# Kernel optimization log

Hardware: AMD Instinct MI355X
Metric: run time of the kernel (lower is better)

The kernel has to match this reference:

```python
import jax, jax.numpy as jnp
import numpy as np


def setup_inputs() -> dict:
    key = jax.random.key(0)
    k1, k2 = jax.random.split(key)
    B, C_IN, C_OUT, K = 256, 1024, 1024, 16
    curr_input = jax.random.normal(k1, (B, C_IN, K), dtype=jnp.float32)
    weight = jax.random.normal(k2, (C_OUT, C_IN, K), dtype=jnp.float32)
    return {"curr_input": curr_input, "weight": weight}


def reference(curr_input, weight):
    # Steady-state streaming conv step:
    # output[b, o] = sum_{c,k} curr_input[b, c, k] * weight[o, c, k]
    # This is exactly the triple nested torch.dot loop, fused into one contraction.
    return jnp.einsum("bck,ock->bo", curr_input, weight)
```

## Files before the change

kernel.cpp:

```cpp
#include <hip/hip_runtime.h>
#include <hip/hip_bf16.h>


#define CO    1024
#define KTOT  16384
#define BM    256
#define BN    128
#define NB    8
#define SKB   64
#define KC    (KTOT / SKB)
#define BK    32
#define KITERS (KC / BK)
#define LDA   40
#define SLICE_ELEMS (BM * CO)

typedef __attribute__((ext_vector_type(8))) short short8;
typedef __attribute__((ext_vector_type(4))) float f32x4;
typedef __attribute__((ext_vector_type(4))) unsigned short u16x4;

__device__ __forceinline__ unsigned short f2bf(float f) {
    union { __bf16 h; unsigned short u; } c; c.h = (__bf16)f; return c.u;
}

__device__ __forceinline__ short8 pack8(f32x4 a, f32x4 b) {
    short8 r;
    r[0] = (short)f2bf(a[0]); r[1] = (short)f2bf(a[1]);
    r[2] = (short)f2bf(a[2]); r[3] = (short)f2bf(a[3]);
    r[4] = (short)f2bf(b[0]); r[5] = (short)f2bf(b[1]);
    r[6] = (short)f2bf(b[2]); r[7] = (short)f2bf(b[3]);
    return r;
}

template <bool USE_WS>
__global__ __launch_bounds__(512, 4)
void sconv_gemm_v8(const float* __restrict__ A, const float* __restrict__ W,
                   float* __restrict__ out, unsigned short* __restrict__ wsb) {
    __shared__ __align__(16) unsigned short lA[2][BM * LDA];
    __shared__ __align__(16) unsigned short lB[2][BN * LDA];

    const int tid  = threadIdx.x;
    const int wid  = tid >> 6;
    const int lane = tid & 63;

    const int wgid = blockIdx.x;
    const int c  = wgid & 7;
    const int rs = wgid >> 3;
    const int nb = rs & 7;
    const int kb = (rs >> 3) * 8 + c;
    const int bn = nb * BN;
    const int k0 = kb * KC;

    const int aR = tid >> 2, aG = tid & 3;
    const int bR = tid >> 2, bG = tid & 3;
    const float* Ap0 = A + (size_t)aR * KTOT + k0 + aG * 8;
    const float* Ap1 = Ap0 + (size_t)128 * KTOT;
    const float* Bp  = W + (size_t)(bn + bR) * KTOT + k0 + bG * 8;
    const int wA0 = aR * LDA + aG * 8;
    const int wA1 = wA0 + 128 * LDA;
    const int wB  = bR * LDA + bG * 8;

#define STAGE(BUF, T) {                                                       \
        f32x4 a00 = *(const f32x4*)(Ap0 + (T) * BK);                          \
        f32x4 a01 = *(const f32x4*)(Ap0 + (T) * BK + 4);                      \
        f32x4 a10 = *(const f32x4*)(Ap1 + (T) * BK);                          \
        f32x4 a11 = *(const f32x4*)(Ap1 + (T) * BK + 4);                      \
        f32x4 b0  = *(const f32x4*)(Bp  + (T) * BK);                          \
        f32x4 b1  = *(const f32x4*)(Bp  + (T) * BK + 4);                      \
        *(short8*)&lA[BUF][wA0] = pack8(a00, a01);                            \
        *(short8*)&lA[BUF][wA1] = pack8(a10, a11);                            \
        *(short8*)&lB[BUF][wB]  = pack8(b0, b1);                              \
    }

    const int wm = (wid >> 1) * 64;
    const int wn = (wid & 1) * 64;
    const int q  = lane >> 4;
    const int fr = lane & 15;

    int offA[4], offB[4];
    #pragma unroll
    for (int mi = 0; mi < 4; ++mi) offA[mi] = (wm + mi * 16 + fr) * LDA + q * 8;
    #pragma unroll
    for (int ni = 0; ni < 4; ++ni) offB[ni] = (wn + ni * 16 + fr) * LDA + q * 8;

    f32x4 acc[4][4] = {};

#define COMPUTE(BUF) {                                                        \
        short8 bf[4];                                                         \
        _Pragma("unroll")                                                     \
        for (int ni = 0; ni < 4; ++ni)                                        \
            bf[ni] = *(const short8*)&lB[BUF][offB[ni]];                      \
        _Pragma("unroll")                                                     \
        for (int mi = 0; mi < 4; ++mi) {                                      \
            short8 af = *(const short8*)&lA[BUF][offA[mi]];                   \
            _Pragma("unroll")                                                 \
            for (int ni = 0; ni < 4; ++ni)                                    \
                acc[mi][ni] = __builtin_amdgcn_mfma_f32_16x16x32_bf16(        \
                    af, bf[ni], acc[mi][ni], 0, 0, 0);                        \
        }                                                                     \
    }

    STAGE(0, 0);
    __syncthreads();
    #pragma unroll
    for (int t = 0; t < KITERS; ++t) {
        COMPUTE(t & 1);
        if (t + 1 < KITERS) STAGE((t + 1) & 1, t + 1);
        __syncthreads();
    }
#undef STAGE
#undef COMPUTE

    if (USE_WS) {
        unsigned short* slice = wsb + (size_t)kb * SLICE_ELEMS;
        const int pbase = bn + wn + fr * 4;
        #pragma unroll
        for (int mi = 0; mi < 4; ++mi) {
            #pragma unroll
            for (int j = 0; j < 4; ++j) {
                const int r = wm + mi * 16 + q * 4 + j;
                u16x4 v;
                #pragma unroll
                for (int ni = 0; ni < 4; ++ni) v[ni] = f2bf(acc[mi][ni][j]);
                *(u16x4*)&slice[(size_t)r * CO + pbase] = v;
            }
        }
    } else {
        #pragma unroll
        for (int mi = 0; mi < 4; ++mi)
            #pragma unroll
            for (int ni = 0; ni < 4; ++ni) {
                const int col = bn + wn + ni * 16 + fr;
                #pragma unroll
                for (int j = 0; j < 4; ++j) {
                    const int r = wm + mi * 16 + q * 4 + j;
                    unsafeAtomicAdd(out + (size_t)r * CO + col, acc[mi][ni][j]);
                }
            }
    }
}

__global__ __launch_bounds__(256)
void reduce_splitk_v8(const unsigned short* __restrict__ ws, float* __restrict__ out) {
    const int g = blockIdx.x * 256 + threadIdx.x;
    const u16x4* base = (const u16x4*)ws;
    float s[4] = {0, 0, 0, 0};
    #pragma unroll 8
    for (int sdx = 0; sdx < SKB; ++sdx) {
        u16x4 v = base[(size_t)sdx * (SLICE_ELEMS / 4) + g];
        #pragma unroll
        for (int e = 0; e < 4; ++e) {
            unsigned int u = ((unsigned int)v[e]) << 16;
            s[e] += __builtin_bit_cast(float, u);
        }
    }
    const int r   = g >> 8;
    const int p   = g & 255;
    const int c64 = p >> 4;
    const int L   = p & 15;
    float* orow = out + (size_t)r * CO + c64 * 64 + L;
    #pragma unroll
    for (int e = 0; e < 4; ++e) orow[e * 16] = s[e];
}

extern "C" void kernel_launch(void* const* d_in, const int* in_sizes, int n_in,
                              void* d_out, int out_size, void* d_ws, size_t ws_size,
                              hipStream_t stream) {
    const float* A = (const float*)d_in[0];
    const float* W = (const float*)d_in[1];
    float* out = (float*)d_out;
    unsigned short* ws = (unsigned short*)d_ws;

    const size_t ws_needed = (size_t)SKB * SLICE_ELEMS * sizeof(unsigned short);

    if (ws_size >= ws_needed) {
        sconv_gemm_v8<true><<<NB * SKB, 512, 0, stream>>>(A, W, out, ws);
        reduce_splitk_v8<<<SLICE_ELEMS / 4 / 256, 256, 0, stream>>>(ws, out);
    } else {
        hipMemsetAsync(d_out, 0, (size_t)out_size * sizeof(float), stream);
        sconv_gemm_v8<false><<<NB * SKB, 512, 0, stream>>>(A, W, out, ws);
    }
}
```

Before: 30.89 us.

## Fuse split-K reduction into GEMM kernel via grid-wide atomic barrier

```diff
diff --git a/kernel.cpp b/kernel.cpp
--- a/kernel.cpp
+++ b/kernel.cpp
@@ -7,7 +7,8 @@
 #define BM    256
 #define BN    128
 #define NB    8
-#define SKB   64
+#define SKB   32
+#define NBLK  (NB * SKB)
 #define KC    (KTOT / SKB)
 #define BK    32
 #define KITERS (KC / BK)
@@ -32,9 +33,10 @@
 }
 
 template <bool USE_WS>
-__global__ __launch_bounds__(512, 4)
-void sconv_gemm_v8(const float* __restrict__ A, const float* __restrict__ W,
-                   float* __restrict__ out, unsigned short* __restrict__ wsb) {
+__global__ __launch_bounds__(512, 2)
+void sconv_fused_v11(const float* __restrict__ A, const float* __restrict__ W,
+                     float* __restrict__ out, unsigned short* __restrict__ slices,
+                     unsigned int* __restrict__ ctr) {
     __shared__ __align__(16) unsigned short lA[2][BM * LDA];
     __shared__ __align__(16) unsigned short lB[2][BN * LDA];
 
@@ -51,13 +53,13 @@
     const int k0 = kb * KC;
 
     const int aR = tid >> 2, aG = tid & 3;
-    const int bR = tid >> 2, bG = tid & 3;
     const float* Ap0 = A + (size_t)aR * KTOT + k0 + aG * 8;
     const float* Ap1 = Ap0 + (size_t)128 * KTOT;
-    const float* Bp  = W + (size_t)(bn + bR) * KTOT + k0 + bG * 8;
     const int wA0 = aR * LDA + aG * 8;
     const int wA1 = wA0 + 128 * LDA;
-    const int wB  = bR * LDA + bG * 8;
+    const int bR = tid >> 2, bG = tid & 3;
+    const float* Bp = W + (size_t)(bn + bR) * KTOT + k0 + bG * 8;
+    const int wB = bR * LDA + bG * 8;
 
 #define STAGE(BUF, T) {                                                       \
         f32x4 a00 = *(const f32x4*)(Ap0 + (T) * BK);                          \
@@ -111,7 +113,7 @@
 #undef COMPUTE
 
     if (USE_WS) {
-        unsigned short* slice = wsb + (size_t)kb * SLICE_ELEMS;
+        unsigned short* slice = slices + (size_t)kb * SLICE_ELEMS;
         const int pbase = bn + wn + fr * 4;
         #pragma unroll
         for (int mi = 0; mi < 4; ++mi) {
@@ -122,6 +124,41 @@
                 #pragma unroll
                 for (int ni = 0; ni < 4; ++ni) v[ni] = f2bf(acc[mi][ni][j]);
                 *(u16x4*)&slice[(size_t)r * CO + pbase] = v;
+            }
+        }
+
+        __threadfence();
+        __syncthreads();
+        if (tid == 0) {
+            __hip_atomic_fetch_add(ctr, 1u, __ATOMIC_ACQ_REL, __HIP_MEMORY_SCOPE_AGENT);
+            while (__hip_atomic_load(ctr, __ATOMIC_ACQUIRE, __HIP_MEMORY_SCOPE_AGENT)
+                   < (unsigned int)NBLK) {
+                __builtin_amdgcn_s_sleep(2);
+            }
+        }
+        __syncthreads();
+
+        if (tid < 256) {
+            const int g = wgid * 256 + tid;
+            const u16x4* base = (const u16x4*)slices;
+            float s[4] = {0, 0, 0, 0};
+            #pragma unroll 8
+            for (int sdx = 0; sdx < SKB; ++sdx) {
+                u16x4 v = base[(size_t)sdx * (SLICE_ELEMS / 4) + g];
+                #pragma unroll
+                for (int e = 0; e < 4; ++e) {
+                    unsigned int u = ((unsigned int)v[e]) << 16;
+                    s[e] += __builtin_bit_cast(float, u);
+                }
+            }
+            #pragma unroll
+            for (int e = 0; e < 4; ++e) {
+                const int f  = g * 4 + e;
+                const int r  = f >> 10;
+                const int cp = f & 1023;
+                const int p  = cp & 63;
+                const int col = (cp & ~63) + (p & 3) * 16 + (p >> 2);
+                out[(size_t)r * CO + col] = s[e];
             }
         }
     } else {
@@ -139,44 +176,22 @@
     }
 }
 
-__global__ __launch_bounds__(256)
-void reduce_splitk_v8(const unsigned short* __restrict__ ws, float* __restrict__ out) {
-    const int g = blockIdx.x * 256 + threadIdx.x;
-    const u16x4* base = (const u16x4*)ws;
-    float s[4] = {0, 0, 0, 0};
-    #pragma unroll 8
-    for (int sdx = 0; sdx < SKB; ++sdx) {
-        u16x4 v = base[(size_t)sdx * (SLICE_ELEMS / 4) + g];
-        #pragma unroll
-        for (int e = 0; e < 4; ++e) {
-            unsigned int u = ((unsigned int)v[e]) << 16;
-            s[e] += __builtin_bit_cast(float, u);
-        }
-    }
-    const int r   = g >> 8;
-    const int p   = g & 255;
-    const int c64 = p >> 4;
-    const int L   = p & 15;
-    float* orow = out + (size_t)r * CO + c64 * 64 + L;
-    #pragma unroll
-    for (int e = 0; e < 4; ++e) orow[e * 16] = s[e];
-}
-
 extern "C" void kernel_launch(void* const* d_in, const int* in_sizes, int n_in,
                               void* d_out, int out_size, void* d_ws, size_t ws_size,
                               hipStream_t stream) {
     const float* A = (const float*)d_in[0];
     const float* W = (const float*)d_in[1];
     float* out = (float*)d_out;
-    unsigned short* ws = (unsigned short*)d_ws;
 
-    const size_t ws_needed = (size_t)SKB * SLICE_ELEMS * sizeof(unsigned short);
+    const size_t ws_needed = 256 + (size_t)SKB * SLICE_ELEMS * sizeof(unsigned short);
 
     if (ws_size >= ws_needed) {
-        sconv_gemm_v8<true><<<NB * SKB, 512, 0, stream>>>(A, W, out, ws);
-        reduce_splitk_v8<<<SLICE_ELEMS / 4 / 256, 256, 0, stream>>>(ws, out);
+        unsigned int*   ctr    = (unsigned int*)d_ws;
+        unsigned short* slices = (unsigned short*)((char*)d_ws + 256);
+        hipMemsetAsync(d_ws, 0, 256, stream);
+        sconv_fused_v11<true><<<NBLK, 512, 0, stream>>>(A, W, out, slices, ctr);
     } else {
         hipMemsetAsync(d_out, 0, (size_t)out_size * sizeof(float), stream);
-        sconv_gemm_v8<false><<<NB * SKB, 512, 0, stream>>>(A, W, out, ws);
+        sconv_fused_v11<false><<<NBLK, 512, 0, stream>>>(A, W, out, nullptr, nullptr);
     }
 }
```

Measured after the change: 105.2 us. 241% more time.

## Split M into two tiles and halve split-K depth, shrinking bf16 partial workspace

Applied to the files above, without the earlier changes.

```diff
diff --git a/kernel.cpp b/kernel.cpp
--- a/kernel.cpp
+++ b/kernel.cpp
@@ -4,15 +4,16 @@
 
 #define CO    1024
 #define KTOT  16384
-#define BM    256
+#define BM    128
 #define BN    128
 #define NB    8
-#define SKB   64
+#define SKB   32
+#define MB    2
 #define KC    (KTOT / SKB)
 #define BK    32
 #define KITERS (KC / BK)
 #define LDA   40
-#define SLICE_ELEMS (BM * CO)
+#define SLICE_ELEMS (256 * CO)
 
 typedef __attribute__((ext_vector_type(8))) short short8;
 typedef __attribute__((ext_vector_type(4))) float f32x4;
@@ -33,8 +34,8 @@
 
 template <bool USE_WS>
 __global__ __launch_bounds__(512, 4)
-void sconv_gemm_v8(const float* __restrict__ A, const float* __restrict__ W,
-                   float* __restrict__ out, unsigned short* __restrict__ wsb) {
+void sconv_gemm_v12(const float* __restrict__ A, const float* __restrict__ W,
+                    float* __restrict__ out, unsigned short* __restrict__ slices) {
     __shared__ __align__(16) unsigned short lA[2][BM * LDA];
     __shared__ __align__(16) unsigned short lB[2][BN * LDA];
 
@@ -45,44 +46,40 @@
     const int wgid = blockIdx.x;
     const int c  = wgid & 7;
     const int rs = wgid >> 3;
-    const int nb = rs & 7;
-    const int kb = (rs >> 3) * 8 + c;
+    const int mb = rs & 1;
+    const int nb = (rs >> 1) & 7;
+    const int kb = (rs >> 4) * 8 + c;
+    const int bm = mb * BM;
     const int bn = nb * BN;
     const int k0 = kb * KC;
 
-    const int aR = tid >> 2, aG = tid & 3;
-    const int bR = tid >> 2, bG = tid & 3;
-    const float* Ap0 = A + (size_t)aR * KTOT + k0 + aG * 8;
-    const float* Ap1 = Ap0 + (size_t)128 * KTOT;
-    const float* Bp  = W + (size_t)(bn + bR) * KTOT + k0 + bG * 8;
-    const int wA0 = aR * LDA + aG * 8;
-    const int wA1 = wA0 + 128 * LDA;
-    const int wB  = bR * LDA + bG * 8;
+    const int sR = tid >> 2, sG = tid & 3;
+    const float* Ap = A + (size_t)(bm + sR) * KTOT + k0 + sG * 8;
+    const float* Bp = W + (size_t)(bn + sR) * KTOT + k0 + sG * 8;
+    const int wAo = sR * LDA + sG * 8;
+    const int wBo = sR * LDA + sG * 8;
 
 #define STAGE(BUF, T) {                                                       \
-        f32x4 a00 = *(const f32x4*)(Ap0 + (T) * BK);                          \
-        f32x4 a01 = *(const f32x4*)(Ap0 + (T) * BK + 4);                      \
-        f32x4 a10 = *(const f32x4*)(Ap1 + (T) * BK);                          \
-        f32x4 a11 = *(const f32x4*)(Ap1 + (T) * BK + 4);                      \
-        f32x4 b0  = *(const f32x4*)(Bp  + (T) * BK);                          \
-        f32x4 b1  = *(const f32x4*)(Bp  + (T) * BK + 4);                      \
-        *(short8*)&lA[BUF][wA0] = pack8(a00, a01);                            \
-        *(short8*)&lA[BUF][wA1] = pack8(a10, a11);                            \
-        *(short8*)&lB[BUF][wB]  = pack8(b0, b1);                              \
+        f32x4 a0 = *(const f32x4*)(Ap + (T) * BK);                            \
+        f32x4 a1 = *(const f32x4*)(Ap + (T) * BK + 4);                        \
+        f32x4 b0 = *(const f32x4*)(Bp + (T) * BK);                            \
+        f32x4 b1 = *(const f32x4*)(Bp + (T) * BK + 4);                        \
+        *(short8*)&lA[BUF][wAo] = pack8(a0, a1);                              \
+        *(short8*)&lB[BUF][wBo] = pack8(b0, b1);                              \
     }
 
-    const int wm = (wid >> 1) * 64;
+    const int wm = (wid >> 1) * 32;
     const int wn = (wid & 1) * 64;
     const int q  = lane >> 4;
     const int fr = lane & 15;
 
-    int offA[4], offB[4];
+    int offA[2], offB[4];
     #pragma unroll
-    for (int mi = 0; mi < 4; ++mi) offA[mi] = (wm + mi * 16 + fr) * LDA + q * 8;
+    for (int mi = 0; mi < 2; ++mi) offA[mi] = (wm + mi * 16 + fr) * LDA + q * 8;
     #pragma unroll
     for (int ni = 0; ni < 4; ++ni) offB[ni] = (wn + ni * 16 + fr) * LDA + q * 8;
 
-    f32x4 acc[4][4] = {};
+    f32x4 acc[2][4] = {};
 
 #define COMPUTE(BUF) {                                                        \
         short8 bf[4];                                                         \
@@ -90,7 +87,7 @@
         for (int ni = 0; ni < 4; ++ni)                                        \
             bf[ni] = *(const short8*)&lB[BUF][offB[ni]];                      \
         _Pragma("unroll")                                                     \
-        for (int mi = 0; mi < 4; ++mi) {                                      \
+        for (int mi = 0; mi < 2; ++mi) {                                      \
             short8 af = *(const short8*)&lA[BUF][offA[mi]];                   \
             _Pragma("unroll")                                                 \
             for (int ni = 0; ni < 4; ++ni)                                    \
@@ -111,13 +108,13 @@
 #undef COMPUTE
 
     if (USE_WS) {
-        unsigned short* slice = wsb + (size_t)kb * SLICE_ELEMS;
+        unsigned short* slice = slices + (size_t)kb * SLICE_ELEMS;
         const int pbase = bn + wn + fr * 4;
         #pragma unroll
-        for (int mi = 0; mi < 4; ++mi) {
+        for (int mi = 0; mi < 2; ++mi) {
             #pragma unroll
             for (int j = 0; j < 4; ++j) {
-                const int r = wm + mi * 16 + q * 4 + j;
+                const int r = bm + wm + mi * 16 + q * 4 + j;
                 u16x4 v;
                 #pragma unroll
                 for (int ni = 0; ni < 4; ++ni) v[ni] = f2bf(acc[mi][ni][j]);
@@ -126,13 +123,13 @@
         }
     } else {
         #pragma unroll
-        for (int mi = 0; mi < 4; ++mi)
+        for (int mi = 0; mi < 2; ++mi)
             #pragma unroll
             for (int ni = 0; ni < 4; ++ni) {
                 const int col = bn + wn + ni * 16 + fr;
                 #pragma unroll
                 for (int j = 0; j < 4; ++j) {
-                    const int r = wm + mi * 16 + q * 4 + j;
+                    const int r = bm + wm + mi * 16 + q * 4 + j;
                     unsafeAtomicAdd(out + (size_t)r * CO + col, acc[mi][ni][j]);
                 }
             }
@@ -140,9 +137,10 @@
 }
 
 __global__ __launch_bounds__(256)
-void reduce_splitk_v8(const unsigned short* __restrict__ ws, float* __restrict__ out) {
+void reduce_splitk_v12(const unsigned short* __restrict__ slices,
+                       float* __restrict__ out) {
     const int g = blockIdx.x * 256 + threadIdx.x;
-    const u16x4* base = (const u16x4*)ws;
+    const u16x4* base = (const u16x4*)slices;
     float s[4] = {0, 0, 0, 0};
     #pragma unroll 8
     for (int sdx = 0; sdx < SKB; ++sdx) {
@@ -153,13 +151,15 @@
             s[e] += __builtin_bit_cast(float, u);
         }
     }
-    const int r   = g >> 8;
-    const int p   = g & 255;
-    const int c64 = p >> 4;
-    const int L   = p & 15;
-    float* orow = out + (size_t)r * CO + c64 * 64 + L;
     #pragma unroll
-    for (int e = 0; e < 4; ++e) orow[e * 16] = s[e];
+    for (int e = 0; e < 4; ++e) {
+        const int f  = g * 4 + e;
+        const int r  = f >> 10;
+        const int cp = f & 1023;
+        const int p  = cp & 63;
+        const int col = (cp & ~63) + (p & 3) * 16 + (p >> 2);
+        out[(size_t)r * CO + col] = s[e];
+    }
 }
 
 extern "C" void kernel_launch(void* const* d_in, const int* in_sizes, int n_in,
@@ -173,10 +173,10 @@
     const size_t ws_needed = (size_t)SKB * SLICE_ELEMS * sizeof(unsigned short);
 
     if (ws_size >= ws_needed) {
-        sconv_gemm_v8<true><<<NB * SKB, 512, 0, stream>>>(A, W, out, ws);
-        reduce_splitk_v8<<<SLICE_ELEMS / 4 / 256, 256, 0, stream>>>(ws, out);
+        sconv_gemm_v12<true><<<NB * SKB * MB, 512, 0, stream>>>(A, W, out, ws);
+        reduce_splitk_v12<<<SLICE_ELEMS / 4 / 256, 256, 0, stream>>>(ws, out);
     } else {
         hipMemsetAsync(d_out, 0, (size_t)out_size * sizeof(float), stream);
-        sconv_gemm_v8<false><<<NB * SKB, 512, 0, stream>>>(A, W, out, ws);
+        sconv_gemm_v12<false><<<NB * SKB * MB, 512, 0, stream>>>(A, W, out, ws);
     }
 }
```

Result: faster. 30.03 us (-2.8%).
